# Optimization experiments

Measured on AMD Instinct MI355X. Metric: run time of the kernel, lower is better.

The kernel has to match this reference:

```python
import jax, jax.numpy as jnp
import numpy as np

B, D_IN, D_HID, D_OUT = 16384, 256, 512, 256
E, K = 8, 2  # expert_num, activate_num


def setup_inputs() -> dict:
    key = jax.random.key(0)
    ks = jax.random.split(key, 6)
    s_in = 1.0 / np.sqrt(D_IN)
    s_hid = 1.0 / np.sqrt(D_HID)
    return {
        "x": jax.random.normal(ks[0], (B, D_IN), dtype=jnp.float32),
        "Wg": jax.random.normal(ks[1], (D_IN, E), dtype=jnp.float32) * s_in,
        "W1": jax.random.normal(ks[2], (E, D_IN, D_HID), dtype=jnp.float32) * s_in,
        "b1": jnp.zeros((E, D_HID), dtype=jnp.float32),
        "W2": jax.random.normal(ks[3], (E, D_HID, D_OUT), dtype=jnp.float32) * s_hid,
        "b2": jnp.zeros((E, D_OUT), dtype=jnp.float32),
    }


def reference(x, Wg, W1, b1, W2, b2):
    # Gating: logits -> top-k -> softmax over the k selected logits.
    # (nn.Dropout on gate logits is identity at inference.)
    gate_logits = x @ Wg                              # [B, E]
    weights, selected = jax.lax.top_k(gate_logits, K)  # [B, K], [B, K]
    weights = jax.nn.softmax(weights.astype(jnp.float32), axis=1).astype(x.dtype)

    # Expert compute, vectorized over experts (same math as the per-expert
    # gather/compute/scatter loop; tokens not routed to expert e get weight 0).
    h = jax.nn.relu(jnp.einsum("bd,edh->ebh", x, W1) + b1[:, None, :])  # [E, B, H]
    expert_out = jnp.einsum("ebh,eho->ebo", h, W2) + b2[:, None, :]      # [E, B, O]

    # Combine weights: combine[b, e] = sum_k weights[b,k] * [selected[b,k]==e]
    one_hot = jax.nn.one_hot(selected, E, dtype=x.dtype)  # [B, K, E]
    combine = jnp.einsum("bk,bke->be", weights, one_hot)  # [B, E]
    results = jnp.einsum("be,ebo->bo", combine, expert_out)  # [B, O]
    return results
```

## Files before the change

### kernel.cpp

```cpp
#include <hip/hip_runtime.h>
#include <hip/hip_bf16.h>

typedef __bf16 bf16x8 __attribute__((ext_vector_type(8)));
typedef __bf16 bf16x4 __attribute__((ext_vector_type(4)));
typedef float f32x4 __attribute__((ext_vector_type(4)));
typedef float f32x16 __attribute__((ext_vector_type(16)));

#define NTOK 16384
#define DIN  256
#define DHID 512
#define DOUT 256
#define NEXP 8

#define MFMA32(a, b, c) __builtin_amdgcn_mfma_f32_32x32x16_bf16(a, b, c, 0, 0, 0)
#define GLD16(gp, lp)                                                       \
  __builtin_amdgcn_global_load_lds(                                         \
      (__attribute__((address_space(1))) void*)(gp),                        \
      (__attribute__((address_space(3))) void*)(lp), 16, 0, 0)

__global__ __launch_bounds__(256) void wcvt_kernel(const float* __restrict__ w1,
                                                   const float* __restrict__ w2,
                                                   __bf16* __restrict__ w1bf,
                                                   __bf16* __restrict__ w2bf) {
  int e = blockIdx.y;
  bool isW1 = blockIdx.x < 64;
  int flat = (isW1 ? blockIdx.x : blockIdx.x - 64) * 256 + threadIdx.x;
  const float* src = isW1 ? w1 : w2;
  __bf16* dst = isW1 ? w1bf : w2bf;
  int K = isW1 ? DIN : DHID;
  int nsh = isW1 ? 9 : 8;
  int N = 1 << nsh;
  int kg = flat >> nsh;
  int n = flat & (N - 1);
  const float* s = src + ((size_t)e * K + (size_t)kg * 8) * N + n;
  bf16x8 t;
#pragma unroll
  for (int j = 0; j < 8; ++j) t[j] = (__bf16)s[(size_t)j * N];
  *(bf16x8*)(dst + (size_t)((e << nsh) + n) * K + kg * 8) = t;
}

__global__ __launch_bounds__(256) void gate_kernel(const float* __restrict__ x,
                                                   const float* __restrict__ wg,
                                                   int* __restrict__ cnt,
                                                   int* __restrict__ btok,
                                                   float* __restrict__ bw,
                                                   __bf16* __restrict__ xbf) {
  __shared__ int lcnt[NEXP];
  __shared__ int lbase[NEXP];
  const int tid = threadIdx.x;
  if (tid < NEXP) lcnt[tid] = 0;

  const int sub = tid & 7;
  const int tslot = tid >> 3;
  const int token = blockIdx.x * 32 + tslot;
  const f32x4* xr = (const f32x4*)(x + (size_t)token * DIN + sub * 32);
  const float* wr0 = wg + (size_t)sub * 32 * NEXP;

  bf16x8 xb[4];
  f32x4 p0 = {0.f, 0.f, 0.f, 0.f}, p1 = {0.f, 0.f, 0.f, 0.f};
#pragma unroll
  for (int j4 = 0; j4 < 8; ++j4) {
    f32x4 xv = xr[j4];
    const float* wr = wr0 + j4 * 32;
#pragma unroll
    for (int d = 0; d < 4; ++d) {
      float xs_ = xv[d];
      p0 += xs_ * *(const f32x4*)(wr + 8 * d);
      p1 += xs_ * *(const f32x4*)(wr + 8 * d + 4);
      xb[j4 >> 1][(j4 & 1) * 4 + d] = (__bf16)xs_;
    }
  }
  {
    bf16x8* xdst = (bf16x8*)(xbf + (size_t)token * DIN + sub * 32);
#pragma unroll
    for (int i = 0; i < 4; ++i) xdst[i] = xb[i];
  }

  double acc[NEXP];
#pragma unroll
  for (int d = 0; d < 4; ++d) {
    acc[d] = (double)p0[d];
    acc[4 + d] = (double)p1[d];
  }
#pragma unroll
  for (int off = 1; off < 8; off <<= 1)
#pragma unroll
    for (int e = 0; e < NEXP; ++e) acc[e] += __shfl_xor(acc[e], off, 64);

  __syncthreads();

  int i1 = 0, i2 = 0, o1 = 0, o2 = 0;
  float w1 = 0.f, w2 = 0.f;
  if (sub == 0) {
    double bv1 = acc[0];
#pragma unroll
    for (int e = 1; e < NEXP; ++e)
      if (acc[e] > bv1) { bv1 = acc[e]; i1 = e; }
    double bv2 = -1e300;
#pragma unroll
    for (int e = 0; e < NEXP; ++e)
      if (e != i1 && acc[e] > bv2) { bv2 = acc[e]; i2 = e; }
    float dd = expf((float)(bv2 - bv1));
    w1 = 1.0f / (1.0f + dd);
    w2 = dd * w1;
    o1 = atomicAdd(&lcnt[i1], 1);
    o2 = atomicAdd(&lcnt[i2], 1);
  }
  __syncthreads();
  if (tid < NEXP) lbase[tid] = atomicAdd(&cnt[tid], lcnt[tid]);
  __syncthreads();
  if (sub == 0) {
    int s1 = lbase[i1] + o1, s2 = lbase[i2] + o2;
    btok[i1 * NTOK + s1] = token;
    bw[i1 * NTOK + s1] = w1;
    btok[i2 * NTOK + s2] = token | 16384;
    bw[i2 * NTOK + s2] = w2;
  }
}

__global__ __launch_bounds__(256, 2) void ffn_kernel(
    const __bf16* __restrict__ xbf, const __bf16* __restrict__ w1bf,
    const __bf16* __restrict__ w2bf, const float* __restrict__ b1g,
    const float* __restrict__ b2g, const int* __restrict__ cnt,
    const int* __restrict__ btok, const float* __restrict__ bw,
    __bf16* __restrict__ pout) {
  __shared__ __align__(16) __bf16 wb1[64 * 256];
  __shared__ __align__(16) __bf16 wb2[256 * 64];
  __shared__ __align__(16) __bf16 hs[64 * 64];
  __shared__ int tok[64];
  __shared__ int srow[64];
  __shared__ float wgt[64];
  __shared__ float b2s[DOUT];

  int b = blockIdx.x;
  int e = -1, start = 0;
  {
    int a0 = 0;
#pragma unroll
    for (int q = 0; q < NEXP; ++q) {
      int t = (cnt[q] + 63) >> 6;
      if (e < 0 && b < a0 + t) { e = q; start = (b - a0) * 64; }
      a0 += t;
    }
  }
  if (e < 0) return;
  const int ce = cnt[e];

  const int tid = threadIdx.x;
  if (tid < 64) {
    int idx = start + tid;
    bool v = idx < ce;
    int entry = v ? btok[e * NTOK + idx] : 0;
    int t = entry & 16383;
    tok[tid] = t;
    srow[tid] = (entry >> 14) * NTOK + t;
    wgt[tid] = v ? bw[e * NTOK + idx] : 0.0f;
  }
  b2s[tid] = b2g[e * DOUT + tid];
  __syncthreads();

  const int lane = tid & 63;
  const int wid = tid >> 6;
  const int hi = lane >> 5;
  const int l31 = lane & 31;
  const int wh = wid >> 1;
  const int wt = wid & 1;
  const int wo = wid;

  bf16x8 xB[16];
  {
    const __bf16* xr = xbf + (size_t)tok[wt * 32 + l31] * DIN + hi * 8;
#pragma unroll
    for (int kw = 0; kw < 16; ++kw) xB[kw] = *(const bf16x8*)(xr + kw * 16);
  }

  const __bf16* w1e = w1bf + (size_t)e * DHID * DIN;
  const __bf16* w2e = w2bf + (size_t)e * DOUT * DHID;

  f32x16 acc[2][2];
#pragma unroll
  for (int ai = 0; ai < 2; ++ai)
#pragma unroll
    for (int bi = 0; bi < 2; ++bi)
#pragma unroll
      for (int r = 0; r < 16; ++r) acc[ai][bi][r] = 0.f;

  for (int hc = 0; hc < 8; ++hc) {
    __syncthreads();

#pragma unroll
    for (int j = 0; j < 8; ++j) {
      int W = wid * 8 + j;
      int n1 = 2 * W + hi;
      int s1 = l31 ^ (n1 & 31);
      GLD16(w1e + (size_t)(hc * 64 + n1) * DIN + s1 * 8, wb1 + W * 512);
      int n2 = 8 * W + (lane >> 3);
      int s2 = (lane & 7) ^ (n2 & 7);
      GLD16(w2e + (size_t)n2 * DHID + hc * 64 + s2 * 8, wb2 + W * 512);
    }
    __syncthreads();

    f32x16 S;
#pragma unroll
    for (int r = 0; r < 16; ++r) S[r] = 0.f;
#pragma unroll
    for (int kw = 0; kw < 16; ++kw) {
      int row = wh * 32 + l31;
      int s = (kw * 2 + hi) ^ (row & 31);
      bf16x8 a = *(const bf16x8*)((const char*)wb1 + row * 512 + s * 16);
      S = MFMA32(a, xB[kw], S);
    }
#pragma unroll
    for (int g = 0; g < 4; ++g) {
      int hl = wh * 32 + 8 * g + 4 * hi;
      f32x4 bv = *(const f32x4*)(b1g + e * DHID + hc * 64 + hl);
      bf16x4 pk;
#pragma unroll
      for (int r = 0; r < 4; ++r)
        pk[r] = (__bf16)fmaxf(S[4 * g + r] + bv[r], 0.f);
      int m = wt * 32 + l31;
      int slot = (hl >> 3) ^ (m & 7);
      *(bf16x4*)((char*)hs + m * 128 + slot * 16 + (hl & 7) * 2) = pk;
    }
    __syncthreads();

#pragma unroll
    for (int kw = 0; kw < 4; ++kw) {
      bf16x8 wf[2], hf[2];
#pragma unroll
      for (int ai = 0; ai < 2; ++ai) {
        int row = wo * 64 + ai * 32 + l31;
        int s = (kw * 2 + hi) ^ (row & 7);
        wf[ai] = *(const bf16x8*)((const char*)wb2 + row * 128 + s * 16);
      }
#pragma unroll
      for (int bi = 0; bi < 2; ++bi) {
        int m = bi * 32 + l31;
        int s = (kw * 2 + hi) ^ (m & 7);
        hf[bi] = *(const bf16x8*)((const char*)hs + m * 128 + s * 16);
      }
      acc[0][0] = MFMA32(wf[0], hf[0], acc[0][0]);
      acc[0][1] = MFMA32(wf[0], hf[1], acc[0][1]);
      acc[1][0] = MFMA32(wf[1], hf[0], acc[1][0]);
      acc[1][1] = MFMA32(wf[1], hf[1], acc[1][1]);
    }
  }

#pragma unroll
  for (int bi = 0; bi < 2; ++bi) {
    int tm = bi * 32 + l31;
    if (start + tm < ce) {
      float wv = wgt[tm];
      __bf16* prow = pout + (size_t)srow[tm] * DOUT;
#pragma unroll
      for (int ai = 0; ai < 2; ++ai) {
#pragma unroll
        for (int g = 0; g < 4; ++g) {
          int o0 = wo * 64 + ai * 32 + 8 * g + 4 * hi;
          f32x4 bv = *(const f32x4*)(&b2s[o0]);
          bf16x4 pk;
#pragma unroll
          for (int r = 0; r < 4; ++r)
            pk[r] = (__bf16)(wv * (acc[ai][bi][4 * g + r] + bv[r]));
          *(bf16x4*)(prow + o0) = pk;
        }
      }
    }
  }
}

__global__ __launch_bounds__(256) void combine_kernel(const __bf16* __restrict__ pout,
                                                      float* __restrict__ out) {
  int f = blockIdx.x * 256 + threadIdx.x;
  bf16x8 a = *(const bf16x8*)(pout + (size_t)f * 8);
  bf16x8 b = *(const bf16x8*)(pout + (size_t)NTOK * DOUT + (size_t)f * 8);
  float4 o0, o1;
  o0.x = (float)a[0] + (float)b[0];
  o0.y = (float)a[1] + (float)b[1];
  o0.z = (float)a[2] + (float)b[2];
  o0.w = (float)a[3] + (float)b[3];
  o1.x = (float)a[4] + (float)b[4];
  o1.y = (float)a[5] + (float)b[5];
  o1.z = (float)a[6] + (float)b[6];
  o1.w = (float)a[7] + (float)b[7];
  float4* dst = (float4*)(out + (size_t)f * 8);
  dst[0] = o0;
  dst[1] = o1;
}

extern "C" void kernel_launch(void* const* d_in, const int* in_sizes, int n_in,
                              void* d_out, int out_size, void* d_ws, size_t ws_size,
                              hipStream_t stream) {
  const float* x = (const float*)d_in[0];
  const float* Wg = (const float*)d_in[1];
  const float* W1 = (const float*)d_in[2];
  const float* b1 = (const float*)d_in[3];
  const float* W2 = (const float*)d_in[4];
  const float* b2 = (const float*)d_in[5];
  float* out = (float*)d_out;

  char* ws = (char*)d_ws;
  int* cnt = (int*)(ws + 0);
  int* btok = (int*)(ws + 256);
  float* bw = (float*)(ws + 524544);
  __bf16* xbf = (__bf16*)(ws + 1048832);
  __bf16* w1bf = (__bf16*)(ws + 9437440);
  __bf16* w2bf = (__bf16*)(ws + 11534592);
  __bf16* pout = (__bf16*)(ws + 13631744);

  hipMemsetAsync(cnt, 0, NEXP * sizeof(int), stream);

  wcvt_kernel<<<dim3(128, NEXP), dim3(256), 0, stream>>>(W1, W2, w1bf, w2bf);
  gate_kernel<<<dim3(NTOK / 32), dim3(256), 0, stream>>>(x, Wg, cnt, btok, bw, xbf);
  ffn_kernel<<<dim3(520), dim3(256), 0, stream>>>(xbf, w1bf, w2bf, b1, b2,
                                                  cnt, btok, bw, pout);
  combine_kernel<<<dim3(NTOK * DOUT / 8 / 256), dim3(256), 0, stream>>>(pout, out);
}
```

Measured before the change: 161.7 us.

## Read W2 fragments directly from pre-packed global layout and prefetch W1 tiles

W2 is repacked at conversion time into an MFMA-fragment-ordered layout, so the FFN kernel loads second-GEMM operands straight from global/L2 into registers instead of staging them through LDS. The W1 tile uses padded LDS rows instead of XOR swizzling and is prefetched for the next hidden chunk after the barrier, overlapping load with the second GEMM. Operand order in the second MFMA is swapped, so the epilogue now writes scalar bf16 values per token rather than packed 4-wide stores, which may cost store efficiency.

```diff
diff --git a/kernel.cpp b/kernel.cpp
--- a/kernel.cpp
+++ b/kernel.cpp
@@ -21,22 +21,27 @@
 __global__ __launch_bounds__(256) void wcvt_kernel(const float* __restrict__ w1,
                                                    const float* __restrict__ w2,
                                                    __bf16* __restrict__ w1bf,
-                                                   __bf16* __restrict__ w2bf) {
+                                                   __bf16* __restrict__ w2p) {
   int e = blockIdx.y;
-  bool isW1 = blockIdx.x < 64;
-  int flat = (isW1 ? blockIdx.x : blockIdx.x - 64) * 256 + threadIdx.x;
-  const float* src = isW1 ? w1 : w2;
-  __bf16* dst = isW1 ? w1bf : w2bf;
-  int K = isW1 ? DIN : DHID;
-  int nsh = isW1 ? 9 : 8;
-  int N = 1 << nsh;
-  int kg = flat >> nsh;
-  int n = flat & (N - 1);
-  const float* s = src + ((size_t)e * K + (size_t)kg * 8) * N + n;
-  bf16x8 t;
-#pragma unroll
-  for (int j = 0; j < 8; ++j) t[j] = (__bf16)s[(size_t)j * N];
-  *(bf16x8*)(dst + (size_t)((e << nsh) + n) * K + kg * 8) = t;
+  if (blockIdx.x < 64) {
+    int flat = blockIdx.x * 256 + threadIdx.x;
+    int kg = flat >> 9;
+    int n = flat & 511;
+    const float* s = w1 + ((size_t)e * 256 + (size_t)kg * 8) * 512 + n;
+    bf16x8 t;
+#pragma unroll
+    for (int j = 0; j < 8; ++j) t[j] = (__bf16)s[(size_t)j * 512];
+    *(bf16x8*)(w1bf + (size_t)(e * 512 + n) * 256 + kg * 8) = t;
+  } else {
+    int flat = (blockIdx.x - 64) * 256 + threadIdx.x;
+    int out = flat & 255;
+    int khigh = flat >> 8;
+    const float* s = w2 + ((size_t)e * 512 + (size_t)khigh * 8) * 256 + out;
+    bf16x8 t;
+#pragma unroll
+    for (int j = 0; j < 8; ++j) t[j] = (__bf16)s[(size_t)j * 256];
+    *(bf16x8*)(w2p + (size_t)e * 131072 + (size_t)flat * 8) = t;
+  }
 }
 
 __global__ __launch_bounds__(256) void gate_kernel(const float* __restrict__ x,
@@ -120,13 +125,12 @@
 
 __global__ __launch_bounds__(256, 2) void ffn_kernel(
     const __bf16* __restrict__ xbf, const __bf16* __restrict__ w1bf,
-    const __bf16* __restrict__ w2bf, const float* __restrict__ b1g,
+    const __bf16* __restrict__ w2p, const float* __restrict__ b1g,
     const float* __restrict__ b2g, const int* __restrict__ cnt,
     const int* __restrict__ btok, const float* __restrict__ bw,
     __bf16* __restrict__ pout) {
-  __shared__ __align__(16) __bf16 wb1[64 * 256];
-  __shared__ __align__(16) __bf16 wb2[256 * 64];
-  __shared__ __align__(16) __bf16 hs[64 * 64];
+  __shared__ __align__(16) __bf16 wb1[64 * 264];
+  __shared__ __align__(16) __bf16 hs[64 * 72];
   __shared__ int tok[64];
   __shared__ int srow[64];
   __shared__ float wgt[64];
@@ -161,11 +165,10 @@
 
   const int lane = tid & 63;
   const int wid = tid >> 6;
+  const int l31 = lane & 31;
   const int hi = lane >> 5;
-  const int l31 = lane & 31;
   const int wh = wid >> 1;
   const int wt = wid & 1;
-  const int wo = wid;
 
   bf16x8 xB[16];
   {
@@ -175,94 +178,88 @@
   }
 
   const __bf16* w1e = w1bf + (size_t)e * DHID * DIN;
-  const __bf16* w2e = w2bf + (size_t)e * DOUT * DHID;
+  const __bf16* w2e = w2p + (size_t)e * 131072;
+
+  auto stage = [&](int hc) {
+    if (lane < 32) {
+#pragma unroll
+      for (int j = 0; j < 16; ++j) {
+        int row = wid * 16 + j;
+        GLD16(w1e + (size_t)(hc * 64 + row) * DIN + l31 * 8,
+              (char*)wb1 + row * 528);
+      }
+    }
+  };
+  stage(0);
 
   f32x16 acc[2][2];
 #pragma unroll
-  for (int ai = 0; ai < 2; ++ai)
-#pragma unroll
-    for (int bi = 0; bi < 2; ++bi)
-#pragma unroll
-      for (int r = 0; r < 16; ++r) acc[ai][bi][r] = 0.f;
+  for (int at = 0; at < 2; ++at)
+#pragma unroll
+    for (int bt = 0; bt < 2; ++bt)
+#pragma unroll
+      for (int r = 0; r < 16; ++r) acc[at][bt][r] = 0.f;
 
   for (int hc = 0; hc < 8; ++hc) {
     __syncthreads();
 
-#pragma unroll
-    for (int j = 0; j < 8; ++j) {
-      int W = wid * 8 + j;
-      int n1 = 2 * W + hi;
-      int s1 = l31 ^ (n1 & 31);
-      GLD16(w1e + (size_t)(hc * 64 + n1) * DIN + s1 * 8, wb1 + W * 512);
-      int n2 = 8 * W + (lane >> 3);
-      int s2 = (lane & 7) ^ (n2 & 7);
-      GLD16(w2e + (size_t)n2 * DHID + hc * 64 + s2 * 8, wb2 + W * 512);
-    }
-    __syncthreads();
-
     f32x16 S;
 #pragma unroll
     for (int r = 0; r < 16; ++r) S[r] = 0.f;
 #pragma unroll
     for (int kw = 0; kw < 16; ++kw) {
       int row = wh * 32 + l31;
-      int s = (kw * 2 + hi) ^ (row & 31);
-      bf16x8 a = *(const bf16x8*)((const char*)wb1 + row * 512 + s * 16);
+      bf16x8 a = *(const bf16x8*)((const char*)wb1 + row * 528 + kw * 32 + hi * 16);
       S = MFMA32(a, xB[kw], S);
     }
 #pragma unroll
-    for (int g = 0; g < 4; ++g) {
-      int hl = wh * 32 + 8 * g + 4 * hi;
+    for (int q = 0; q < 4; ++q) {
+      int hl = wh * 32 + q * 8 + hi * 4;
       f32x4 bv = *(const f32x4*)(b1g + e * DHID + hc * 64 + hl);
       bf16x4 pk;
 #pragma unroll
       for (int r = 0; r < 4; ++r)
-        pk[r] = (__bf16)fmaxf(S[4 * g + r] + bv[r], 0.f);
+        pk[r] = (__bf16)fmaxf(S[4 * q + r] + bv[r], 0.f);
       int m = wt * 32 + l31;
-      int slot = (hl >> 3) ^ (m & 7);
-      *(bf16x4*)((char*)hs + m * 128 + slot * 16 + (hl & 7) * 2) = pk;
+      *(bf16x4*)((char*)hs + m * 144 + hl * 2) = pk;
     }
     __syncthreads();
 
+    if (hc < 7) stage(hc + 1);
+
 #pragma unroll
     for (int kw = 0; kw < 4; ++kw) {
-      bf16x8 wf[2], hf[2];
-#pragma unroll
-      for (int ai = 0; ai < 2; ++ai) {
-        int row = wo * 64 + ai * 32 + l31;
-        int s = (kw * 2 + hi) ^ (row & 7);
-        wf[ai] = *(const bf16x8*)((const char*)wb2 + row * 128 + s * 16);
-      }
-#pragma unroll
-      for (int bi = 0; bi < 2; ++bi) {
-        int m = bi * 32 + l31;
-        int s = (kw * 2 + hi) ^ (m & 7);
-        hf[bi] = *(const bf16x8*)((const char*)hs + m * 128 + s * 16);
-      }
-      acc[0][0] = MFMA32(wf[0], hf[0], acc[0][0]);
-      acc[0][1] = MFMA32(wf[0], hf[1], acc[0][1]);
-      acc[1][0] = MFMA32(wf[1], hf[0], acc[1][0]);
-      acc[1][1] = MFMA32(wf[1], hf[1], acc[1][1]);
-    }
-  }
-
-#pragma unroll
-  for (int bi = 0; bi < 2; ++bi) {
-    int tm = bi * 32 + l31;
-    if (start + tm < ce) {
-      float wv = wgt[tm];
-      __bf16* prow = pout + (size_t)srow[tm] * DOUT;
-#pragma unroll
-      for (int ai = 0; ai < 2; ++ai) {
-#pragma unroll
-        for (int g = 0; g < 4; ++g) {
-          int o0 = wo * 64 + ai * 32 + 8 * g + 4 * hi;
-          f32x4 bv = *(const f32x4*)(&b2s[o0]);
-          bf16x4 pk;
-#pragma unroll
-          for (int r = 0; r < 4; ++r)
-            pk[r] = (__bf16)(wv * (acc[ai][bi][4 * g + r] + bv[r]));
-          *(bf16x4*)(prow + o0) = pk;
+      bf16x8 hf[2], wf[2];
+#pragma unroll
+      for (int bt = 0; bt < 2; ++bt)
+        hf[bt] = *(const bf16x8*)((const char*)hs + (bt * 32 + l31) * 144 +
+                                  kw * 32 + hi * 16);
+#pragma unroll
+      for (int at = 0; at < 2; ++at)
+        wf[at] = *(const bf16x8*)(w2e + (size_t)(hc * 4 + kw) * 4096 +
+                                  hi * 2048 + (wid * 64 + at * 32 + l31) * 8);
+      acc[0][0] = MFMA32(hf[0], wf[0], acc[0][0]);
+      acc[0][1] = MFMA32(hf[1], wf[0], acc[0][1]);
+      acc[1][0] = MFMA32(hf[0], wf[1], acc[1][0]);
+      acc[1][1] = MFMA32(hf[1], wf[1], acc[1][1]);
+    }
+  }
+
+#pragma unroll
+  for (int at = 0; at < 2; ++at) {
+    int outc = wid * 64 + at * 32 + l31;
+    float b2v = b2s[outc];
+#pragma unroll
+    for (int bt = 0; bt < 2; ++bt) {
+#pragma unroll
+      for (int q = 0; q < 4; ++q) {
+#pragma unroll
+        for (int r = 0; r < 4; ++r) {
+          int tokr = bt * 32 + q * 8 + hi * 4 + r;
+          if (start + tokr < ce) {
+            float v = wgt[tokr] * (acc[at][bt][4 * q + r] + b2v);
+            pout[(size_t)srow[tokr] * DOUT + outc] = (__bf16)v;
+          }
         }
       }
     }
@@ -305,14 +302,14 @@
   float* bw = (float*)(ws + 524544);
   __bf16* xbf = (__bf16*)(ws + 1048832);
   __bf16* w1bf = (__bf16*)(ws + 9437440);
-  __bf16* w2bf = (__bf16*)(ws + 11534592);
+  __bf16* w2p = (__bf16*)(ws + 11534592);
   __bf16* pout = (__bf16*)(ws + 13631744);
 
   hipMemsetAsync(cnt, 0, NEXP * sizeof(int), stream);
 
-  wcvt_kernel<<<dim3(128, NEXP), dim3(256), 0, stream>>>(W1, W2, w1bf, w2bf);
+  wcvt_kernel<<<dim3(128, NEXP), dim3(256), 0, stream>>>(W1, W2, w1bf, w2p);
   gate_kernel<<<dim3(NTOK / 32), dim3(256), 0, stream>>>(x, Wg, cnt, btok, bw, xbf);
-  ffn_kernel<<<dim3(520), dim3(256), 0, stream>>>(xbf, w1bf, w2bf, b1, b2,
+  ffn_kernel<<<dim3(520), dim3(256), 0, stream>>>(xbf, w1bf, w2p, b1, b2,
                                                   cnt, btok, bw, pout);
   combine_kernel<<<dim3(NTOK * DOUT / 8 / 256), dim3(256), 0, stream>>>(pout, out);
 }
```

Measured after the change: 170.6 us. 5.5% more time.

## Merge weight conversion into gating kernel and interleave expert tiles in FFN

Applied to the files above, without the earlier changes.

Folds the weight-conversion kernel into the gating kernel, with extra blocks handling W1/W2 bf16 transposes, which removes one launch and lets the two jobs overlap. The FFN kernel now assigns experts round-robin by blockIdx (e = bid & 7) and each block loops over that expert's 64-token tiles with stride 64, replacing the prefix-sum block-to-expert mapping, and the grid shrinks from 520 to 512 blocks. Placing the experts side by side is meant to spread weight traffic and balance the load, but an expert with more than 64 tiles makes some blocks run several tiles one after another, which can cause tail imbalance.

```diff
diff --git a/kernel.cpp b/kernel.cpp
--- a/kernel.cpp
+++ b/kernel.cpp
@@ -18,41 +18,47 @@
       (__attribute__((address_space(1))) void*)(gp),                        \
       (__attribute__((address_space(3))) void*)(lp), 16, 0, 0)
 
-__global__ __launch_bounds__(256) void wcvt_kernel(const float* __restrict__ w1,
-                                                   const float* __restrict__ w2,
-                                                   __bf16* __restrict__ w1bf,
-                                                   __bf16* __restrict__ w2bf) {
-  int e = blockIdx.y;
-  bool isW1 = blockIdx.x < 64;
-  int flat = (isW1 ? blockIdx.x : blockIdx.x - 64) * 256 + threadIdx.x;
-  const float* src = isW1 ? w1 : w2;
-  __bf16* dst = isW1 ? w1bf : w2bf;
-  int K = isW1 ? DIN : DHID;
-  int nsh = isW1 ? 9 : 8;
-  int N = 1 << nsh;
-  int kg = flat >> nsh;
-  int n = flat & (N - 1);
-  const float* s = src + ((size_t)e * K + (size_t)kg * 8) * N + n;
-  bf16x8 t;
-#pragma unroll
-  for (int j = 0; j < 8; ++j) t[j] = (__bf16)s[(size_t)j * N];
-  *(bf16x8*)(dst + (size_t)((e << nsh) + n) * K + kg * 8) = t;
-}
-
-__global__ __launch_bounds__(256) void gate_kernel(const float* __restrict__ x,
-                                                   const float* __restrict__ wg,
-                                                   int* __restrict__ cnt,
-                                                   int* __restrict__ btok,
-                                                   float* __restrict__ bw,
-                                                   __bf16* __restrict__ xbf) {
+__global__ __launch_bounds__(256) void prep_kernel(
+    const float* __restrict__ x, const float* __restrict__ wg,
+    const float* __restrict__ w1, const float* __restrict__ w2,
+    int* __restrict__ cnt, int* __restrict__ btok, float* __restrict__ bw,
+    __bf16* __restrict__ xbf, __bf16* __restrict__ w1bf,
+    __bf16* __restrict__ w2bf) {
   __shared__ int lcnt[NEXP];
   __shared__ int lbase[NEXP];
+  const int b = blockIdx.x;
   const int tid = threadIdx.x;
+
+  if (b >= 512) {
+    if (b < 1024) {
+      int e = (b - 512) >> 6;
+      int flat = ((b - 512) & 63) * 256 + tid;
+      int kg = flat >> 9;
+      int n = flat & 511;
+      const float* s = w1 + ((size_t)e * 256 + (size_t)kg * 8) * 512 + n;
+      bf16x8 t;
+#pragma unroll
+      for (int j = 0; j < 8; ++j) t[j] = (__bf16)s[(size_t)j * 512];
+      *(bf16x8*)(w1bf + (size_t)(e * 512 + n) * 256 + kg * 8) = t;
+    } else {
+      int e = (b - 1024) >> 6;
+      int flat = ((b - 1024) & 63) * 256 + tid;
+      int kg = flat >> 8;
+      int n = flat & 255;
+      const float* s = w2 + ((size_t)e * 512 + (size_t)kg * 8) * 256 + n;
+      bf16x8 t;
+#pragma unroll
+      for (int j = 0; j < 8; ++j) t[j] = (__bf16)s[(size_t)j * 256];
+      *(bf16x8*)(w2bf + (size_t)(e * 256 + n) * 512 + kg * 8) = t;
+    }
+    return;
+  }
+
   if (tid < NEXP) lcnt[tid] = 0;
 
   const int sub = tid & 7;
   const int tslot = tid >> 3;
-  const int token = blockIdx.x * 32 + tslot;
+  const int token = b * 32 + tslot;
   const f32x4* xr = (const f32x4*)(x + (size_t)token * DIN + sub * 32);
   const float* wr0 = wg + (size_t)sub * 32 * NEXP;
 
@@ -90,7 +96,7 @@
   __syncthreads();
 
   int i1 = 0, i2 = 0, o1 = 0, o2 = 0;
-  float w1 = 0.f, w2 = 0.f;
+  float w1s = 0.f, w2s = 0.f;
   if (sub == 0) {
     double bv1 = acc[0];
 #pragma unroll
@@ -101,8 +107,8 @@
     for (int e = 0; e < NEXP; ++e)
       if (e != i1 && acc[e] > bv2) { bv2 = acc[e]; i2 = e; }
     float dd = expf((float)(bv2 - bv1));
-    w1 = 1.0f / (1.0f + dd);
-    w2 = dd * w1;
+    w1s = 1.0f / (1.0f + dd);
+    w2s = dd * w1s;
     o1 = atomicAdd(&lcnt[i1], 1);
     o2 = atomicAdd(&lcnt[i2], 1);
   }
@@ -112,9 +118,9 @@
   if (sub == 0) {
     int s1 = lbase[i1] + o1, s2 = lbase[i2] + o2;
     btok[i1 * NTOK + s1] = token;
-    bw[i1 * NTOK + s1] = w1;
+    bw[i1 * NTOK + s1] = w1s;
     btok[i2 * NTOK + s2] = token | 16384;
-    bw[i2 * NTOK + s2] = w2;
+    bw[i2 * NTOK + s2] = w2s;
   }
 }
 
@@ -132,32 +138,13 @@
   __shared__ float wgt[64];
   __shared__ float b2s[DOUT];
 
-  int b = blockIdx.x;
-  int e = -1, start = 0;
-  {
-    int a0 = 0;
-#pragma unroll
-    for (int q = 0; q < NEXP; ++q) {
-      int t = (cnt[q] + 63) >> 6;
-      if (e < 0 && b < a0 + t) { e = q; start = (b - a0) * 64; }
-      a0 += t;
-    }
-  }
-  if (e < 0) return;
+  const int e = blockIdx.x & 7;
+  const int slot = blockIdx.x >> 3;
   const int ce = cnt[e];
+  const int nt = (ce + 63) >> 6;
 
   const int tid = threadIdx.x;
-  if (tid < 64) {
-    int idx = start + tid;
-    bool v = idx < ce;
-    int entry = v ? btok[e * NTOK + idx] : 0;
-    int t = entry & 16383;
-    tok[tid] = t;
-    srow[tid] = (entry >> 14) * NTOK + t;
-    wgt[tid] = v ? bw[e * NTOK + idx] : 0.0f;
-  }
   b2s[tid] = b2g[e * DOUT + tid];
-  __syncthreads();
 
   const int lane = tid & 63;
   const int wid = tid >> 6;
@@ -167,102 +154,118 @@
   const int wt = wid & 1;
   const int wo = wid;
 
-  bf16x8 xB[16];
-  {
-    const __bf16* xr = xbf + (size_t)tok[wt * 32 + l31] * DIN + hi * 8;
-#pragma unroll
-    for (int kw = 0; kw < 16; ++kw) xB[kw] = *(const bf16x8*)(xr + kw * 16);
-  }
-
   const __bf16* w1e = w1bf + (size_t)e * DHID * DIN;
   const __bf16* w2e = w2bf + (size_t)e * DOUT * DHID;
 
-  f32x16 acc[2][2];
-#pragma unroll
-  for (int ai = 0; ai < 2; ++ai)
-#pragma unroll
-    for (int bi = 0; bi < 2; ++bi)
-#pragma unroll
-      for (int r = 0; r < 16; ++r) acc[ai][bi][r] = 0.f;
-
-  for (int hc = 0; hc < 8; ++hc) {
+  for (int t = slot; t < nt; t += 64) {
+    const int start = t * 64;
     __syncthreads();
 
-#pragma unroll
-    for (int j = 0; j < 8; ++j) {
-      int W = wid * 8 + j;
-      int n1 = 2 * W + hi;
-      int s1 = l31 ^ (n1 & 31);
-      GLD16(w1e + (size_t)(hc * 64 + n1) * DIN + s1 * 8, wb1 + W * 512);
-      int n2 = 8 * W + (lane >> 3);
-      int s2 = (lane & 7) ^ (n2 & 7);
-      GLD16(w2e + (size_t)n2 * DHID + hc * 64 + s2 * 8, wb2 + W * 512);
+    if (tid < 64) {
+      int idx = start + tid;
+      bool v = idx < ce;
+      int entry = v ? btok[e * NTOK + idx] : 0;
+      int tk = entry & 16383;
+      tok[tid] = tk;
+      srow[tid] = (entry >> 14) * NTOK + tk;
+      wgt[tid] = v ? bw[e * NTOK + idx] : 0.0f;
     }
     __syncthreads();
 
-    f32x16 S;
-#pragma unroll
-    for (int r = 0; r < 16; ++r) S[r] = 0.f;
-#pragma unroll
-    for (int kw = 0; kw < 16; ++kw) {
-      int row = wh * 32 + l31;
-      int s = (kw * 2 + hi) ^ (row & 31);
-      bf16x8 a = *(const bf16x8*)((const char*)wb1 + row * 512 + s * 16);
-      S = MFMA32(a, xB[kw], S);
-    }
-#pragma unroll
-    for (int g = 0; g < 4; ++g) {
-      int hl = wh * 32 + 8 * g + 4 * hi;
-      f32x4 bv = *(const f32x4*)(b1g + e * DHID + hc * 64 + hl);
-      bf16x4 pk;
-#pragma unroll
-      for (int r = 0; r < 4; ++r)
-        pk[r] = (__bf16)fmaxf(S[4 * g + r] + bv[r], 0.f);
-      int m = wt * 32 + l31;
-      int slot = (hl >> 3) ^ (m & 7);
-      *(bf16x4*)((char*)hs + m * 128 + slot * 16 + (hl & 7) * 2) = pk;
-    }
-    __syncthreads();
-
-#pragma unroll
-    for (int kw = 0; kw < 4; ++kw) {
-      bf16x8 wf[2], hf[2];
-#pragma unroll
-      for (int ai = 0; ai < 2; ++ai) {
-        int row = wo * 64 + ai * 32 + l31;
-        int s = (kw * 2 + hi) ^ (row & 7);
-        wf[ai] = *(const bf16x8*)((const char*)wb2 + row * 128 + s * 16);
-      }
-#pragma unroll
-      for (int bi = 0; bi < 2; ++bi) {
-        int m = bi * 32 + l31;
-        int s = (kw * 2 + hi) ^ (m & 7);
-        hf[bi] = *(const bf16x8*)((const char*)hs + m * 128 + s * 16);
-      }
-      acc[0][0] = MFMA32(wf[0], hf[0], acc[0][0]);
-      acc[0][1] = MFMA32(wf[0], hf[1], acc[0][1]);
-      acc[1][0] = MFMA32(wf[1], hf[0], acc[1][0]);
-      acc[1][1] = MFMA32(wf[1], hf[1], acc[1][1]);
-    }
-  }
-
-#pragma unroll
-  for (int bi = 0; bi < 2; ++bi) {
-    int tm = bi * 32 + l31;
-    if (start + tm < ce) {
-      float wv = wgt[tm];
-      __bf16* prow = pout + (size_t)srow[tm] * DOUT;
-#pragma unroll
-      for (int ai = 0; ai < 2; ++ai) {
-#pragma unroll
-        for (int g = 0; g < 4; ++g) {
-          int o0 = wo * 64 + ai * 32 + 8 * g + 4 * hi;
-          f32x4 bv = *(const f32x4*)(&b2s[o0]);
-          bf16x4 pk;
-#pragma unroll
-          for (int r = 0; r < 4; ++r)
-            pk[r] = (__bf16)(wv * (acc[ai][bi][4 * g + r] + bv[r]));
-          *(bf16x4*)(prow + o0) = pk;
+    bf16x8 xB[16];
+    {
+      const __bf16* xr = xbf + (size_t)tok[wt * 32 + l31] * DIN + hi * 8;
+#pragma unroll
+      for (int kw = 0; kw < 16; ++kw) xB[kw] = *(const bf16x8*)(xr + kw * 16);
+    }
+
+    f32x16 acc[2][2];
+#pragma unroll
+    for (int ai = 0; ai < 2; ++ai)
+#pragma unroll
+      for (int bi = 0; bi < 2; ++bi)
+#pragma unroll
+        for (int r = 0; r < 16; ++r) acc[ai][bi][r] = 0.f;
+
+    for (int hc = 0; hc < 8; ++hc) {
+      __syncthreads();
+
+#pragma unroll
+      for (int j = 0; j < 8; ++j) {
+        int W = wid * 8 + j;
+        int n1 = 2 * W + hi;
+        int s1 = l31 ^ (n1 & 31);
+        GLD16(w1e + (size_t)(hc * 64 + n1) * DIN + s1 * 8, wb1 + W * 512);
+        int n2 = 8 * W + (lane >> 3);
+        int s2 = (lane & 7) ^ (n2 & 7);
+        GLD16(w2e + (size_t)n2 * DHID + hc * 64 + s2 * 8, wb2 + W * 512);
+      }
+      __syncthreads();
+
+      f32x16 S;
+#pragma unroll
+      for (int r = 0; r < 16; ++r) S[r] = 0.f;
+#pragma unroll
+      for (int kw = 0; kw < 16; ++kw) {
+        int row = wh * 32 + l31;
+        int s = (kw * 2 + hi) ^ (row & 31);
+        bf16x8 a = *(const bf16x8*)((const char*)wb1 + row * 512 + s * 16);
+        S = MFMA32(a, xB[kw], S);
+      }
+#pragma unroll
+      for (int g = 0; g < 4; ++g) {
+        int hl = wh * 32 + 8 * g + 4 * hi;
+        f32x4 bv = *(const f32x4*)(b1g + e * DHID + hc * 64 + hl);
+        bf16x4 pk;
+#pragma unroll
+        for (int r = 0; r < 4; ++r)
+          pk[r] = (__bf16)fmaxf(S[4 * g + r] + bv[r], 0.f);
+        int m = wt * 32 + l31;
+        int slt = (hl >> 3) ^ (m & 7);
+        *(bf16x4*)((char*)hs + m * 128 + slt * 16 + (hl & 7) * 2) = pk;
+      }
+      __syncthreads();
+
+#pragma unroll
+      for (int kw = 0; kw < 4; ++kw) {
+        bf16x8 wf[2], hf[2];
+#pragma unroll
+        for (int ai = 0; ai < 2; ++ai) {
+          int row = wo * 64 + ai * 32 + l31;
+          int s = (kw * 2 + hi) ^ (row & 7);
+          wf[ai] = *(const bf16x8*)((const char*)wb2 + row * 128 + s * 16);
+        }
+#pragma unroll
+        for (int bi = 0; bi < 2; ++bi) {
+          int m = bi * 32 + l31;
+          int s = (kw * 2 + hi) ^ (m & 7);
+          hf[bi] = *(const bf16x8*)((const char*)hs + m * 128 + s * 16);
+        }
+        acc[0][0] = MFMA32(wf[0], hf[0], acc[0][0]);
+        acc[0][1] = MFMA32(wf[0], hf[1], acc[0][1]);
+        acc[1][0] = MFMA32(wf[1], hf[0], acc[1][0]);
+        acc[1][1] = MFMA32(wf[1], hf[1], acc[1][1]);
+      }
+    }
+
+#pragma unroll
+    for (int bi = 0; bi < 2; ++bi) {
+      int tm = bi * 32 + l31;
+      if (start + tm < ce) {
+        float wv = wgt[tm];
+        __bf16* prow = pout + (size_t)srow[tm] * DOUT;
+#pragma unroll
+        for (int ai = 0; ai < 2; ++ai) {
+#pragma unroll
+          for (int g = 0; g < 4; ++g) {
+            int o0 = wo * 64 + ai * 32 + 8 * g + 4 * hi;
+            f32x4 bv = *(const f32x4*)(&b2s[o0]);
+            bf16x4 pk;
+#pragma unroll
+            for (int r = 0; r < 4; ++r)
+              pk[r] = (__bf16)(wv * (acc[ai][bi][4 * g + r] + bv[r]));
+            *(bf16x4*)(prow + o0) = pk;
+          }
         }
       }
     }
@@ -310,9 +313,9 @@
 
   hipMemsetAsync(cnt, 0, NEXP * sizeof(int), stream);
 
-  wcvt_kernel<<<dim3(128, NEXP), dim3(256), 0, stream>>>(W1, W2, w1bf, w2bf);
-  gate_kernel<<<dim3(NTOK / 32), dim3(256), 0, stream>>>(x, Wg, cnt, btok, bw, xbf);
-  ffn_kernel<<<dim3(520), dim3(256), 0, stream>>>(xbf, w1bf, w2bf, b1, b2,
+  prep_kernel<<<dim3(1536), dim3(256), 0, stream>>>(x, Wg, W1, W2, cnt, btok,
+                                                    bw, xbf, w1bf, w2bf);
+  ffn_kernel<<<dim3(512), dim3(256), 0, stream>>>(xbf, w1bf, w2bf, b1, b2,
                                                   cnt, btok, bw, pout);
   combine_kernel<<<dim3(NTOK * DOUT / 8 / 256), dim3(256), 0, stream>>>(pout, out);
 }
```

Result: slower. 166.4 us (+2.9%).
